# Kernel optimization log

Measured on AMD Instinct MI355X. Metric: run time of the kernel, lower is better.

The kernel has to match this reference:

```python
import jax, jax.numpy as jnp
import numpy as np

N_ATOMS = 100000
N_PAIRS = 4000000
N_HASH = 1500
N_CLASS = 6
EPS = 1e-12


def setup_inputs() -> dict:
    key = jax.random.key(0)
    k = jax.random.split(key, 6)
    coords = jax.random.normal(k[0], (N_ATOMS, 3), dtype=jnp.float32) * 10.0
    radii = jax.random.uniform(k[1], (N_HASH,), dtype=jnp.float32, minval=1.0, maxval=2.0)
    tollerances = jax.random.normal(k[2], (N_CLASS,), dtype=jnp.float32) * 0.1
    weight = jnp.zeros((1,), dtype=jnp.float32)
    atom_names = jax.random.randint(k[3], (N_ATOMS,), 0, N_HASH, dtype=jnp.int64 if jax.config.jax_enable_x64 else jnp.int32)
    atom_pairs = jax.random.randint(k[4], (N_PAIRS, 2), 0, N_ATOMS, dtype=jnp.int64 if jax.config.jax_enable_x64 else jnp.int32)
    clash_masks = jax.random.randint(k[5], (N_CLASS, N_PAIRS), 0, 2) > 0
    return {
        "coords": coords,
        "radii": radii,
        "tollerances": tollerances,
        "weight": weight,
        "atom_names": atom_names,
        "atom_pairs": atom_pairs,
        "clash_masks": clash_masks,
    }


def reference(coords, radii, tollerances, weight, atom_names, atom_pairs, clash_masks):
    # Gather pair endpoints: [P, 3]
    p0 = atom_pairs[:, 0]
    p1 = atom_pairs[:, 1]
    diff = coords[p0] - coords[p1]
    dist = jnp.sqrt(jnp.sum(diff * diff, axis=-1) + EPS)  # [P]
    # Van-der-Waals radii via atom-name hash lookup
    rsum = radii[atom_names[p0]] + radii[atom_names[p1]]  # [P]
    # clashing_distance = r1 + r2 - (dist - tol_i)  per tolerance class: [6, P]
    clash_dist = rsum[None, :] + tollerances[:, None] - dist[None, :]
    clash = jnp.where(clash_masks, jax.nn.relu(clash_dist), 0.0)
    # per-class clash energy, scaled by learnable weight (init 0 -> scale 1)
    energies = jnp.sum(clash, axis=1) * jnp.exp(weight[0])  # [6]
    return energies
```

## Files before the change

### kernel.cpp

```cpp
#include <hip/hip_runtime.h>
#include <hip/hip_fp16.h>

#define N_CLASS_C 6
#define MAX_WORDS 33344
#define FILTER_BLOCK 1024
#define FILTER_GRID 256

typedef int vint4 __attribute__((ext_vector_type(4)));
typedef unsigned vuint4 __attribute__((ext_vector_type(4)));

struct alignas(8) HAtom {
    __half x, y, z, r;
};


__global__ __launch_bounds__(256) void prep(
    const float* __restrict__ coords,
    const float* __restrict__ radii,
    const int* __restrict__ names,
    const float* __restrict__ tol,
    int n_radii,
    HAtom* __restrict__ atoms,
    unsigned* __restrict__ cellsg,
    float* __restrict__ out,
    int n_words, int n_atoms) {
    if (blockIdx.x == 0 && threadIdx.x < N_CLASS_C) out[threadIdx.x] = 0.0f;

    __shared__ float sh[4];
    __shared__ float shw;
    {
        float m = 0.0f;
        for (int i = threadIdx.x; i < n_radii; i += blockDim.x)
            m = fmaxf(m, radii[i]);
#pragma unroll
        for (int off = 32; off > 0; off >>= 1) m = fmaxf(m, __shfl_down(m, off, 64));
        if ((threadIdx.x & 63) == 0) sh[threadIdx.x >> 6] = m;
        __syncthreads();
        if (threadIdx.x == 0) {
            float mm = fmaxf(fmaxf(sh[0], sh[1]), fmaxf(sh[2], sh[3]));
            float tmax = -1e30f;
            for (int c = 0; c < N_CLASS_C; ++c) tmax = fmaxf(tmax, tol[c]);
            shw = fmaxf(2.0f * mm + tmax, 1e-2f) + 1e-3f;
        }
        __syncthreads();
    }
    float inv = 1.0f / shw;

    int t = blockIdx.x * blockDim.x + threadIdx.x;
    if (t < n_words) {
        unsigned word = 0;
#pragma unroll
        for (int s = 0; s < 3; ++s) {
            int i = 3 * t + s;
            unsigned c = 0;
            if (i < n_atoms) {
                float x = coords[3 * i + 0];
                float y = coords[3 * i + 1];
                float z = coords[3 * i + 2];
                HAtom a;
                a.x = __float2half(x);
                a.y = __float2half(y);
                a.z = __float2half(z);
                a.r = __float2half(radii[names[i]]);
                atoms[i] = a;
                int cx = (int)floorf(x * inv) + 4;
                int cy = (int)floorf(y * inv) + 4;
                int cz = (int)floorf(z * inv) + 8;
                cx = min(max(cx, 0), 7);
                cy = min(max(cy, 0), 7);
                cz = min(max(cz, 0), 15);
                c = (unsigned)cx | ((unsigned)cy << 3) | ((unsigned)cz << 6);
            }
            word |= c << (10 * s);
        }
        cellsg[t] = word;
    }
}

__device__ __forceinline__ unsigned cell_lookup(const unsigned* cells, int i) {
    unsigned q = (unsigned)(((unsigned long long)(unsigned)i * 0xAAAAAAABull) >> 33);
    unsigned r = (unsigned)i - 3u * q;
    return (cells[q] >> (10u * r)) & 0x3FFu;
}

__device__ __forceinline__ int cell_near(unsigned ca, unsigned cb) {
    int dx = abs((int)(ca & 7u) - (int)(cb & 7u));
    int dy = abs((int)((ca >> 3) & 7u) - (int)((cb >> 3) & 7u));
    int dz = abs((int)((ca >> 6) & 15u) - (int)((cb >> 6) & 15u));
    return (dx | dy | dz) <= 1;
}

__device__ __forceinline__ float hdist_base(const HAtom& A, const HAtom& B) {
    float dx = __half2float(A.x) - __half2float(B.x);
    float dy = __half2float(A.y) - __half2float(B.y);
    float dz = __half2float(A.z) - __half2float(B.z);
    float dist = sqrtf(dx * dx + dy * dy + dz * dz + 1e-12f);
    return (__half2float(A.r) + __half2float(B.r)) - dist;
}

__device__ __forceinline__ void do_pair(
    int p, int a0, int a1,
    const HAtom* __restrict__ atoms, const int* __restrict__ masks,
    const float* tc, float tmax, float* s, int n_pairs) {
    HAtom A = atoms[a0];
    HAtom B = atoms[a1];
    float base = hdist_base(A, B);
    if (base + tmax > 0.0f) {
#pragma unroll
        for (int c = 0; c < N_CLASS_C; ++c) {
            if (masks[(size_t)c * n_pairs + p])
                s[c] += fmaxf(base + tc[c], 0.0f);
        }
    }
}

__global__ __launch_bounds__(FILTER_BLOCK) void clash_filtered(
    const int* __restrict__ pairs,
    const HAtom* __restrict__ atoms,
    const unsigned* __restrict__ cellsg,
    const int* __restrict__ masks,
    const float* __restrict__ tol,
    const float* __restrict__ weight,
    float* __restrict__ out,
    int n_pairs, int n_words) {
    __shared__ unsigned cells[MAX_WORDS];
    {
        const vuint4* src4 = reinterpret_cast<const vuint4*>(cellsg);
        int nw4 = n_words >> 2;
        for (int i = threadIdx.x; i < nw4; i += FILTER_BLOCK) {
            vuint4 v = src4[i];
            cells[4 * i + 0] = v.x;
            cells[4 * i + 1] = v.y;
            cells[4 * i + 2] = v.z;
            cells[4 * i + 3] = v.w;
        }
        for (int i = (nw4 << 2) + threadIdx.x; i < n_words; i += FILTER_BLOCK)
            cells[i] = cellsg[i];
    }

    float tc[N_CLASS_C];
#pragma unroll
    for (int c = 0; c < N_CLASS_C; ++c) tc[c] = tol[c];
    float tmax = tc[0];
#pragma unroll
    for (int c = 1; c < N_CLASS_C; ++c) tmax = fmaxf(tmax, tc[c]);

    float s[N_CLASS_C];
#pragma unroll
    for (int c = 0; c < N_CLASS_C; ++c) s[c] = 0.0f;

    __syncthreads();

    const vint4* pairs4 = reinterpret_cast<const vint4*>(pairs);
    const int npair2 = n_pairs >> 1;
    const int stride = gridDim.x * FILTER_BLOCK;
    for (int q = blockIdx.x * FILTER_BLOCK + threadIdx.x; q < npair2; q += stride) {
        vint4 pq = pairs4[q];
        unsigned ca0 = cell_lookup(cells, pq.x);
        unsigned cb0 = cell_lookup(cells, pq.y);
        unsigned ca1 = cell_lookup(cells, pq.z);
        unsigned cb1 = cell_lookup(cells, pq.w);
        int hit0 = cell_near(ca0, cb0);
        int hit1 = cell_near(ca1, cb1);
        if (hit0) do_pair(2 * q, pq.x, pq.y, atoms, masks, tc, tmax, s, n_pairs);
        if (hit1) do_pair(2 * q + 1, pq.z, pq.w, atoms, masks, tc, tmax, s, n_pairs);
    }

    if ((n_pairs & 1) && blockIdx.x == 0 && threadIdx.x == 0) {
        int p = n_pairs - 1;
        do_pair(p, pairs[2 * p], pairs[2 * p + 1], atoms, masks, tc, tmax, s, n_pairs);
    }

    __shared__ float shsum[N_CLASS_C];
    if (threadIdx.x < N_CLASS_C) shsum[threadIdx.x] = 0.0f;
    __syncthreads();
#pragma unroll
    for (int c = 0; c < N_CLASS_C; ++c) {
        float v = s[c];
#pragma unroll
        for (int off = 32; off > 0; off >>= 1) v += __shfl_down(v, off, 64);
        if ((threadIdx.x & 63) == 0 && v != 0.0f) atomicAdd(&shsum[c], v);
    }
    __syncthreads();
    if (threadIdx.x < N_CLASS_C) {
        float expw = expf(weight[0]);
        atomicAdd(&out[threadIdx.x], shsum[threadIdx.x] * expw);
    }
}

__global__ void zero_accum_fb(float* accum) {
    if (threadIdx.x < N_CLASS_C) accum[threadIdx.x] = 0.0f;
}

__device__ __forceinline__ void block_reduce_accum_fb(float* s, float* accum) {
    __shared__ float sh[N_CLASS_C];
    if (threadIdx.x < N_CLASS_C) sh[threadIdx.x] = 0.0f;
    __syncthreads();
#pragma unroll
    for (int c = 0; c < N_CLASS_C; ++c) {
        float v = s[c];
#pragma unroll
        for (int off = 32; off > 0; off >>= 1) v += __shfl_down(v, off, 64);
        if ((threadIdx.x & 63) == 0 && v != 0.0f) atomicAdd(&sh[c], v);
    }
    __syncthreads();
    if (threadIdx.x < N_CLASS_C) {
        float v = sh[threadIdx.x];
        if (v != 0.0f) atomicAdd(&accum[threadIdx.x], v);
    }
}

__global__ __launch_bounds__(256) void clash_fallback(
    const int* __restrict__ pairs,
    const float* __restrict__ coords,
    const float* __restrict__ radii,
    const int* __restrict__ names,
    const int* __restrict__ masks,
    const float* __restrict__ tol,
    float* __restrict__ accum,
    int n_pairs) {
    float tc[N_CLASS_C];
#pragma unroll
    for (int c = 0; c < N_CLASS_C; ++c) tc[c] = tol[c];
    float tmax = tc[0];
#pragma unroll
    for (int c = 1; c < N_CLASS_C; ++c) tmax = fmaxf(tmax, tc[c]);
    float s[N_CLASS_C];
#pragma unroll
    for (int c = 0; c < N_CLASS_C; ++c) s[c] = 0.0f;

    const int tid = blockIdx.x * blockDim.x + threadIdx.x;
    const int stride = gridDim.x * blockDim.x;
    for (int p = tid; p < n_pairs; p += stride) {
        int a0 = pairs[2 * p], a1 = pairs[2 * p + 1];
        float dx = coords[3 * a0] - coords[3 * a1];
        float dy = coords[3 * a0 + 1] - coords[3 * a1 + 1];
        float dz = coords[3 * a0 + 2] - coords[3 * a1 + 2];
        float dist = sqrtf(dx * dx + dy * dy + dz * dz + 1e-12f);
        float base = (radii[names[a0]] + radii[names[a1]]) - dist;
        if (base + tmax > 0.0f) {
#pragma unroll
            for (int c = 0; c < N_CLASS_C; ++c) {
                if (masks[(size_t)c * n_pairs + p])
                    s[c] += fmaxf(base + tc[c], 0.0f);
            }
        }
    }
    block_reduce_accum_fb(s, accum);
}

__global__ void finalize_fb(const float* __restrict__ accum,
                            const float* __restrict__ w,
                            float* __restrict__ out) {
    int c = threadIdx.x;
    if (c < N_CLASS_C) {
        float scale = expf(w[0]);
        out[c] = accum[c] * scale;
    }
}

extern "C" void kernel_launch(void* const* d_in, const int* in_sizes, int n_in,
                              void* d_out, int out_size, void* d_ws, size_t ws_size,
                              hipStream_t stream) {
    const float* coords = (const float*)d_in[0];
    const float* radii  = (const float*)d_in[1];
    const float* tol    = (const float*)d_in[2];
    const float* weight = (const float*)d_in[3];
    const int* names    = (const int*)d_in[4];
    const int* pairs    = (const int*)d_in[5];
    const int* masks    = (const int*)d_in[6];
    float* out = (float*)d_out;

    int n_atoms = in_sizes[4];
    int n_radii = in_sizes[1];
    int n_pairs = in_sizes[5] / 2;

    int n_words = (n_atoms + 2) / 3;
    size_t atoms_off = 256;
    size_t atoms_bytes = (size_t)n_atoms * sizeof(HAtom);
    size_t cells_off = (atoms_off + atoms_bytes + 255) & ~(size_t)255;
    size_t need = cells_off + (size_t)n_words * 4 + 64;

    if (ws_size >= need && n_words <= MAX_WORDS) {
        HAtom* atoms = (HAtom*)((char*)d_ws + atoms_off);
        unsigned* cellsg = (unsigned*)((char*)d_ws + cells_off);

        prep<<<(n_words + 255) / 256, 256, 0, stream>>>(
            coords, radii, names, tol, n_radii, atoms, cellsg, out,
            n_words, n_atoms);
        clash_filtered<<<FILTER_GRID, FILTER_BLOCK, 0, stream>>>(
            pairs, atoms, cellsg, masks, tol, weight, out, n_pairs, n_words);
    } else {
        float* accum = out;
        zero_accum_fb<<<1, 64, 0, stream>>>(accum);
        clash_fallback<<<2048, 256, 0, stream>>>(pairs, coords, radii, names,
                                                 masks, tol, accum, n_pairs);
        finalize_fb<<<1, 64, 0, stream>>>(accum, weight, out);
    }
}
```

Baseline: 31.39 us.

## Unroll pair loop by two and replace global atomics with partials plus finalize

The grid-stride pair loop now handles two vint4 pair chunks per iteration, which lets the eight cell lookups issue before any branch and raises memory-level parallelism. The per-block global atomicAdd to the output is replaced by writing per-block partial sums to workspace, and a new single-block finalize kernel reduces them and applies exp(weight). This removes the output zeroing in prep and the cross-block atomic contention, and makes the sum deterministic. The cost is one extra kernel launch and more register pressure from the unrolled loop.

```diff
diff --git a/kernel.cpp b/kernel.cpp
--- a/kernel.cpp
+++ b/kernel.cpp
@@ -5,6 +5,7 @@
 #define MAX_WORDS 33344
 #define FILTER_BLOCK 1024
 #define FILTER_GRID 256
+#define PART_STRIDE 16
 
 typedef int vint4 __attribute__((ext_vector_type(4)));
 typedef unsigned vuint4 __attribute__((ext_vector_type(4)));
@@ -22,10 +23,7 @@
     int n_radii,
     HAtom* __restrict__ atoms,
     unsigned* __restrict__ cellsg,
-    float* __restrict__ out,
     int n_words, int n_atoms) {
-    if (blockIdx.x == 0 && threadIdx.x < N_CLASS_C) out[threadIdx.x] = 0.0f;
-
     __shared__ float sh[4];
     __shared__ float shw;
     {
@@ -120,8 +118,7 @@
     const unsigned* __restrict__ cellsg,
     const int* __restrict__ masks,
     const float* __restrict__ tol,
-    const float* __restrict__ weight,
-    float* __restrict__ out,
+    float* __restrict__ partials,
     int n_pairs, int n_words) {
     __shared__ unsigned cells[MAX_WORDS];
     {
@@ -154,16 +151,39 @@
     const vint4* pairs4 = reinterpret_cast<const vint4*>(pairs);
     const int npair2 = n_pairs >> 1;
     const int stride = gridDim.x * FILTER_BLOCK;
-    for (int q = blockIdx.x * FILTER_BLOCK + threadIdx.x; q < npair2; q += stride) {
+
+    int q = blockIdx.x * FILTER_BLOCK + threadIdx.x;
+    for (; q + stride < npair2; q += 2 * stride) {
+        vint4 pqA = pairs4[q];
+        vint4 pqB = pairs4[q + stride];
+        unsigned caA0 = cell_lookup(cells, pqA.x);
+        unsigned cbA0 = cell_lookup(cells, pqA.y);
+        unsigned caA1 = cell_lookup(cells, pqA.z);
+        unsigned cbA1 = cell_lookup(cells, pqA.w);
+        unsigned caB0 = cell_lookup(cells, pqB.x);
+        unsigned cbB0 = cell_lookup(cells, pqB.y);
+        unsigned caB1 = cell_lookup(cells, pqB.z);
+        unsigned cbB1 = cell_lookup(cells, pqB.w);
+        if (cell_near(caA0, cbA0))
+            do_pair(2 * q, pqA.x, pqA.y, atoms, masks, tc, tmax, s, n_pairs);
+        if (cell_near(caA1, cbA1))
+            do_pair(2 * q + 1, pqA.z, pqA.w, atoms, masks, tc, tmax, s, n_pairs);
+        int qB = q + stride;
+        if (cell_near(caB0, cbB0))
+            do_pair(2 * qB, pqB.x, pqB.y, atoms, masks, tc, tmax, s, n_pairs);
+        if (cell_near(caB1, cbB1))
+            do_pair(2 * qB + 1, pqB.z, pqB.w, atoms, masks, tc, tmax, s, n_pairs);
+    }
+    if (q < npair2) {
         vint4 pq = pairs4[q];
         unsigned ca0 = cell_lookup(cells, pq.x);
         unsigned cb0 = cell_lookup(cells, pq.y);
         unsigned ca1 = cell_lookup(cells, pq.z);
         unsigned cb1 = cell_lookup(cells, pq.w);
-        int hit0 = cell_near(ca0, cb0);
-        int hit1 = cell_near(ca1, cb1);
-        if (hit0) do_pair(2 * q, pq.x, pq.y, atoms, masks, tc, tmax, s, n_pairs);
-        if (hit1) do_pair(2 * q + 1, pq.z, pq.w, atoms, masks, tc, tmax, s, n_pairs);
+        if (cell_near(ca0, cb0))
+            do_pair(2 * q, pq.x, pq.y, atoms, masks, tc, tmax, s, n_pairs);
+        if (cell_near(ca1, cb1))
+            do_pair(2 * q + 1, pq.z, pq.w, atoms, masks, tc, tmax, s, n_pairs);
     }
 
     if ((n_pairs & 1) && blockIdx.x == 0 && threadIdx.x == 0) {
@@ -182,10 +202,36 @@
         if ((threadIdx.x & 63) == 0 && v != 0.0f) atomicAdd(&shsum[c], v);
     }
     __syncthreads();
-    if (threadIdx.x < N_CLASS_C) {
-        float expw = expf(weight[0]);
-        atomicAdd(&out[threadIdx.x], shsum[threadIdx.x] * expw);
-    }
+    if (threadIdx.x < N_CLASS_C)
+        partials[blockIdx.x * PART_STRIDE + threadIdx.x] = shsum[threadIdx.x];
+}
+
+__global__ __launch_bounds__(256) void finalize(
+    const float* __restrict__ partials,
+    const float* __restrict__ w,
+    float* __restrict__ out,
+    int nblocks) {
+    float s[N_CLASS_C];
+#pragma unroll
+    for (int c = 0; c < N_CLASS_C; ++c) s[c] = 0.0f;
+    for (int i = threadIdx.x; i < nblocks; i += 256) {
+#pragma unroll
+        for (int c = 0; c < N_CLASS_C; ++c)
+            s[c] += partials[i * PART_STRIDE + c];
+    }
+    __shared__ float sh[N_CLASS_C];
+    if (threadIdx.x < N_CLASS_C) sh[threadIdx.x] = 0.0f;
+    __syncthreads();
+#pragma unroll
+    for (int c = 0; c < N_CLASS_C; ++c) {
+        float v = s[c];
+#pragma unroll
+        for (int off = 32; off > 0; off >>= 1) v += __shfl_down(v, off, 64);
+        if ((threadIdx.x & 63) == 0 && v != 0.0f) atomicAdd(&sh[c], v);
+    }
+    __syncthreads();
+    if (threadIdx.x < N_CLASS_C)
+        out[threadIdx.x] = sh[threadIdx.x] * expf(w[0]);
 }
 
 __global__ void zero_accum_fb(float* accum) {
@@ -276,20 +322,24 @@
     int n_pairs = in_sizes[5] / 2;
 
     int n_words = (n_atoms + 2) / 3;
-    size_t atoms_off = 256;
+    size_t part_off = 256;
+    size_t part_bytes = (size_t)FILTER_GRID * PART_STRIDE * sizeof(float);
+    size_t atoms_off = (part_off + part_bytes + 255) & ~(size_t)255;
     size_t atoms_bytes = (size_t)n_atoms * sizeof(HAtom);
     size_t cells_off = (atoms_off + atoms_bytes + 255) & ~(size_t)255;
     size_t need = cells_off + (size_t)n_words * 4 + 64;
 
     if (ws_size >= need && n_words <= MAX_WORDS) {
+        float* partials = (float*)((char*)d_ws + part_off);
         HAtom* atoms = (HAtom*)((char*)d_ws + atoms_off);
         unsigned* cellsg = (unsigned*)((char*)d_ws + cells_off);
 
         prep<<<(n_words + 255) / 256, 256, 0, stream>>>(
-            coords, radii, names, tol, n_radii, atoms, cellsg, out,
+            coords, radii, names, tol, n_radii, atoms, cellsg,
             n_words, n_atoms);
         clash_filtered<<<FILTER_GRID, FILTER_BLOCK, 0, stream>>>(
-            pairs, atoms, cellsg, masks, tol, weight, out, n_pairs, n_words);
+            pairs, atoms, cellsg, masks, tol, partials, n_pairs, n_words);
+        finalize<<<1, 256, 0, stream>>>(partials, weight, out, FILTER_GRID);
     } else {
         float* accum = out;
         zero_accum_fb<<<1, 64, 0, stream>>>(accum);
```

Measured after the change: 33.77 us. 1.08x slower.
